# Kernel tuning notes

Hardware: AMD Instinct MI355X
Metric: run time of the kernel (lower is better)

## Reference

```python
import jax, jax.numpy as jnp
import numpy as np
import math

B, S, T = 32, 128, 64
FEAT = 16
H = 1024
V = 32000


def _gru_step(x, h, wih, whh, bih, bhh):
    # torch nn.GRU cell: gates ordered (r, z, n)
    gi = x @ wih.T + bih
    gh = h @ whh.T + bhh
    ir, iz, in_ = jnp.split(gi, 3, axis=-1)
    hr, hz, hn = jnp.split(gh, 3, axis=-1)
    r = jax.nn.sigmoid(ir + hr)
    z = jax.nn.sigmoid(iz + hz)
    n = jnp.tanh(in_ + r * hn)
    return (1.0 - z) * n + z * h


def _forward(features, target_tokens, temp_W, temp_b, hum_W, hum_b, cloud_W, cloud_b,
             time_W, time_b, other_W, other_b, fi_W, fi_b,
             enc_wih, enc_whh, enc_bih, enc_bhh, emb, attn_W, attn_b,
             dec_wih, dec_whh, dec_bih, dec_bhh, out_W, out_b):
    b = features.shape[0]
    # per-feature projections (dropout = identity in eval mode)
    temp = features[:, :, 0:1] @ temp_W.T + temp_b
    hum = features[:, :, 1:2] @ hum_W.T + hum_b
    cloud = features[:, :, 2:3] @ cloud_W.T + cloud_b
    time = features[:, :, -5:-3] @ time_W.T + time_b
    other_in = jnp.concatenate([features[:, :, 3:-5], features[:, :, -3:]], axis=2)
    other = other_in @ other_W.T + other_b
    concat = jnp.concatenate([temp, hum, cloud, time, other], axis=2)  # [B,S,2H]
    proj = jnp.tanh(concat @ fi_W.T + fi_b)  # [B,S,H]

    # encoder GRU over time
    def enc_step(h, x):
        h2 = _gru_step(x, h, enc_wih, enc_whh, enc_bih, enc_bhh)
        return h2, h2
    h0 = jnp.zeros((b, H), proj.dtype)
    h_last, enc_outs = jax.lax.scan(enc_step, h0, proj.transpose(1, 0, 2))
    enc_out = enc_outs.transpose(1, 0, 2)  # [B,S,H]

    # attention keys computed once (loop-invariant in the original)
    keys = enc_out @ attn_W.T + attn_b  # [B,S,H]
    scale = 1.0 / math.sqrt(H)

    # decoder: teacher_forcing_ratio = 1.0 -> input at step t is target_tokens[:, t-1]
    def dec_step(h, tok):
        e = emb[tok]  # [B,H]
        scores = jnp.einsum('bh,bsh->bs', h, keys) * scale
        w = jax.nn.softmax(scores, axis=-1)
        ctx = jnp.einsum('bs,bsh->bh', w, enc_out)
        x = jnp.concatenate([e, ctx], axis=-1)  # [B,2H]
        h2 = _gru_step(x, h, dec_wih, dec_whh, dec_bih, dec_bhh)
        pred = jnp.concatenate([h2, ctx], axis=-1) @ out_W.T + out_b  # [B,V]
        return h2, pred

    _, preds = jax.lax.scan(dec_step, h_last, target_tokens[:, :-1].T)  # [T-1,B,V]
    outputs = jnp.zeros((b, target_tokens.shape[1], V), preds.dtype)
    outputs = outputs.at[:, 0, target_tokens[0, 0]].set(1.0)
    outputs = outputs.at[:, 1:, :].set(preds.transpose(1, 0, 2))
    return outputs


def setup_inputs() -> dict:
    key = jax.random.key(0)
    ks = jax.random.split(key, 32)
    nrm = lambda k, sh: jax.random.normal(k, sh, jnp.float32) * 0.05
    Hq = H // 4
    d = {}
    d['features'] = jax.random.normal(ks[0], (B, S, FEAT), jnp.float32)
    d['target_tokens'] = jax.random.randint(ks[1], (B, T), 0, V, dtype=jnp.int32)
    d['temp_W'] = nrm(ks[2], (Hq, 1)); d['temp_b'] = nrm(ks[3], (Hq,))
    d['hum_W'] = nrm(ks[4], (Hq, 1)); d['hum_b'] = nrm(ks[5], (Hq,))
    d['cloud_W'] = nrm(ks[6], (Hq, 1)); d['cloud_b'] = nrm(ks[7], (Hq,))
    d['time_W'] = nrm(ks[8], (Hq, 2)); d['time_b'] = nrm(ks[9], (Hq,))
    d['other_W'] = nrm(ks[10], (H, FEAT - 5)); d['other_b'] = nrm(ks[11], (H,))
    d['fi_W'] = nrm(ks[12], (H, 2 * H)); d['fi_b'] = nrm(ks[13], (H,))
    d['enc_wih'] = nrm(ks[14], (3 * H, H)); d['enc_whh'] = nrm(ks[15], (3 * H, H))
    d['enc_bih'] = nrm(ks[16], (3 * H,)); d['enc_bhh'] = nrm(ks[17], (3 * H,))
    d['emb'] = nrm(ks[18], (V, H))
    d['attn_W'] = nrm(ks[19], (H, H)); d['attn_b'] = nrm(ks[20], (H,))
    d['dec_wih'] = nrm(ks[21], (3 * H, 2 * H)); d['dec_whh'] = nrm(ks[22], (3 * H, H))
    d['dec_bih'] = nrm(ks[23], (3 * H,)); d['dec_bhh'] = nrm(ks[24], (3 * H,))
    d['out_W'] = nrm(ks[25], (V, 2 * H)); d['out_b'] = nrm(ks[26], (V,))
    return d


def reference(features, target_tokens, temp_W, temp_b, hum_W, hum_b, cloud_W, cloud_b,
              time_W, time_b, other_W, other_b, fi_W, fi_b,
              enc_wih, enc_whh, enc_bih, enc_bhh, emb, attn_W, attn_b,
              dec_wih, dec_whh, dec_bih, dec_bhh, out_W, out_b):
    return _forward(features, target_tokens, temp_W, temp_b, hum_W, hum_b, cloud_W, cloud_b,
                    time_W, time_b, other_W, other_b, fi_W, fi_b,
                    enc_wih, enc_whh, enc_bih, enc_bhh, emb, attn_W, attn_b,
                    dec_wih, dec_whh, dec_bih, dec_bhh, out_W, out_b)
```

## Files before the change

### kernel.cpp

```cpp
#include <hip/hip_runtime.h>

typedef float f32x4 __attribute__((ext_vector_type(4)));
typedef __bf16 bf16x8 __attribute__((ext_vector_type(8)));

#define DI static __device__ __forceinline__

DI unsigned short f2bf(float f) {
  unsigned u = __float_as_uint(f);
  u = (u + 0x7fffu + ((u >> 16) & 1u)) >> 16;
  return (unsigned short)u;
}
DI unsigned pk2(float lo, float hi) {
  return (unsigned)f2bf(lo) | ((unsigned)f2bf(hi) << 16);
}
DI float bflo(unsigned u) { return __uint_as_float(u << 16); }
DI float bfhi(unsigned u) { return __uint_as_float(u & 0xffff0000u); }
DI float sigm(float x) { return 1.0f / (1.0f + expf(-x)); }

DI void gl_lds16(const unsigned short* g, unsigned short* l) {
  __builtin_amdgcn_global_load_lds(
      (const __attribute__((address_space(1))) unsigned int*)g,
      (__attribute__((address_space(3))) unsigned int*)l, 16, 0, 0);
}

DI void st32_sc1(unsigned* p, unsigned v) {
  __hip_atomic_store(p, v, __ATOMIC_RELAXED, __HIP_MEMORY_SCOPE_AGENT);
}
DI void st64_sc1(unsigned long long* p, unsigned long long v) {
  __hip_atomic_store(p, v, __ATOMIC_RELAXED, __HIP_MEMORY_SCOPE_AGENT);
}
DI int ldw(const int* p) {
  return __hip_atomic_load(p, __ATOMIC_RELAXED, __HIP_MEMORY_SCOPE_AGENT);
}
DI void stw(int* p, int v) {
  __hip_atomic_store(p, v, __ATOMIC_RELAXED, __HIP_MEMORY_SCOPE_AGENT);
}

DI void burn(int n) {
  float x = (float)(int)threadIdx.x;
#pragma unroll 1
  for (int i = 0; i < n; ++i) x = __builtin_fmaf(x, 1.0000001f, 1e-9f);
  asm volatile("" :: "v"(x));
}

DI void waitrel(const int* relbase, int repl, int target) {
  const int* w = relbase + repl * 32;
  for (;;) {
    int v = 0;
    if ((threadIdx.x & 63) == 0) v = ldw(w);
    v = __shfl(v, 0);
    if (v >= target) break;
    burn(60);
  }
  asm volatile("" ::: "memory");
}
DI void strel(int* relbase, int v) {
  int l = threadIdx.x & 63;
  if (l < 8) stw(relbase + l * 32, v);
}

__global__ void k_fold(const float* __restrict__ tW, const float* __restrict__ tb,
                       const float* __restrict__ hW, const float* __restrict__ hb,
                       const float* __restrict__ cW, const float* __restrict__ cb,
                       const float* __restrict__ tiW, const float* __restrict__ tib,
                       const float* __restrict__ oW, const float* __restrict__ ob,
                       const float* __restrict__ fiW, const float* __restrict__ fib,
                       float* __restrict__ M, float* __restrict__ b0v)
{
  int g = blockIdx.x * 256 + threadIdx.x;
  if (g >= 1024 * 17) return;
  int h = g / 17, f = g - h * 17;
  const float* fw = fiW + (size_t)h * 2048;
  float s = 0.f;
  if (f == 16) {
    for (int k = 0; k < 256; ++k) s += fw[k] * tb[k];
    for (int k = 0; k < 256; ++k) s += fw[256 + k] * hb[k];
    for (int k = 0; k < 256; ++k) s += fw[512 + k] * cb[k];
    for (int k = 0; k < 256; ++k) s += fw[768 + k] * tib[k];
    for (int r = 0; r < 1024; ++r) s += fw[1024 + r] * ob[r];
    b0v[h] = s + fib[h];
  } else if (f == 0) {
    for (int k = 0; k < 256; ++k) s += fw[k] * tW[k];
    M[h * 16 + 0] = s;
  } else if (f == 1) {
    for (int k = 0; k < 256; ++k) s += fw[256 + k] * hW[k];
    M[h * 16 + 1] = s;
  } else if (f == 2) {
    for (int k = 0; k < 256; ++k) s += fw[512 + k] * cW[k];
    M[h * 16 + 2] = s;
  } else if (f == 11) {
    for (int k = 0; k < 256; ++k) s += fw[768 + k] * tiW[2 * k];
    M[h * 16 + 11] = s;
  } else if (f == 12) {
    for (int k = 0; k < 256; ++k) s += fw[768 + k] * tiW[2 * k + 1];
    M[h * 16 + 12] = s;
  } else {
    int col = (f <= 10) ? (f - 3) : (f - 5);
    for (int r = 0; r < 1024; ++r) s += fw[1024 + r] * oW[r * 11 + col];
    M[h * 16 + f] = s;
  }
}

__global__ __launch_bounds__(256)
void k_proj(const float* __restrict__ feat, const float* __restrict__ M,
            const float* __restrict__ b0v, unsigned short* __restrict__ proj)
{
  __shared__ float ft[16];
  int bs = blockIdx.x;
  int h = blockIdx.y * 256 + threadIdx.x;
  if (threadIdx.x < 16) ft[threadIdx.x] = feat[bs * 16 + threadIdx.x];
  __syncthreads();
  float sum = b0v[h];
  const float* mr = M + h * 16;
#pragma unroll
  for (int f = 0; f < 16; ++f) sum += mr[f] * ft[f];
  proj[(size_t)bs * 1024 + h] = f2bf(tanhf(sum));
}

__global__ void k_conv(const float* __restrict__ s, unsigned short* __restrict__ d, int n8)
{
  for (long i = (long)blockIdx.x * 256 + threadIdx.x; i < n8; i += (long)gridDim.x * 256) {
    const float* p = s + i * 8;
    f32x4 a = *(const f32x4*)p, b = *(const f32x4*)(p + 4);
    uint4 o;
    o.x = pk2(a[0], a[1]); o.y = pk2(a[2], a[3]);
    o.z = pk2(b[0], b[1]); o.w = pk2(b[2], b[3]);
    *(uint4*)(d + i * 8) = o;
  }
}

__global__ void k_conv_str(const float* __restrict__ s, unsigned short* __restrict__ d, int coff)
{
  int r = blockIdx.x;
  int c = threadIdx.x * 4;
  f32x4 a = *(const f32x4*)(s + (size_t)r * 2048 + coff + c);
  uint2 o; o.x = pk2(a[0], a[1]); o.y = pk2(a[2], a[3]);
  *(uint2*)(d + (size_t)r * 1024 + c) = o;
}

__global__ void k_gather_e(const int* __restrict__ toks, const float* __restrict__ emb,
                           unsigned short* __restrict__ e_bf)
{
  int row = blockIdx.x;
  int t = row >> 5, b = row & 31;
  unsigned short* dst = e_bf + (size_t)row * 1024 + threadIdx.x * 4;
  if (t < 63) {
    int tok = toks[b * 64 + t];
    f32x4 a = *(const f32x4*)(emb + (size_t)tok * 1024 + threadIdx.x * 4);
    uint2 o; o.x = pk2(a[0], a[1]); o.y = pk2(a[2], a[3]);
    *(uint2*)dst = o;
  } else {
    uint2 o; o.x = 0u; o.y = 0u;
    *(uint2*)dst = o;
  }
}

__global__ void k_onehot(const int* __restrict__ toks, float* __restrict__ out)
{
  int i = blockIdx.x * 256 + threadIdx.x;
  if (i >= 32 * 32000) return;
  int b = i / 32000, v = i - b * 32000;
  out[(size_t)b * 64 * 32000 + v] = (v == toks[0]) ? 1.0f : 0.0f;
}

template<int MODE>
__global__ __launch_bounds__(256)
void gemm_bf(const unsigned short* __restrict__ A, const unsigned short* __restrict__ B,
             const float* __restrict__ bias, float* __restrict__ Cf,
             unsigned short* __restrict__ Cb,
             int tiles_m, int K, int lda, int ldb, int ldc, int coloff)
{
  __shared__ unsigned short As[4096];
  __shared__ unsigned short Bs[4096];
  const int nblk = gridDim.x;
  const int cpx = nblk >> 3;
  const int bid = blockIdx.x;
  const int id = (bid & 7) * cpx + (bid >> 3);
  const int tm = id % tiles_m, tn = id / tiles_m;
  const int tid = threadIdx.x;
  const int lane = tid & 63, wave = tid >> 6;
  const int wm = (wave & 1) << 6, wn = (wave >> 1) << 6;
  const int r0 = tid >> 2, kc0 = (tid & 3) << 3;
  const unsigned short* ga0 = A + (size_t)(tm * 128 + r0) * lda + kc0;
  const unsigned short* ga1 = A + (size_t)(tm * 128 + 64 + r0) * lda + kc0;
  const unsigned short* gb0 = B + (size_t)(tn * 128 + r0) * ldb + kc0;
  const unsigned short* gb1 = B + (size_t)(tn * 128 + 64 + r0) * ldb + kc0;
  const int lr = lane & 15, lkb = (lane >> 4) << 3;

  f32x4 acc[4][4];
#pragma unroll
  for (int m = 0; m < 4; ++m)
#pragma unroll
    for (int n = 0; n < 4; ++n) { acc[m][n][0]=0.f; acc[m][n][1]=0.f; acc[m][n][2]=0.f; acc[m][n][3]=0.f; }

  for (int kt = 0; kt < K; kt += 32) {
    __syncthreads();
    gl_lds16(ga0 + kt, &As[tid * 8]);
    gl_lds16(ga1 + kt, &As[(tid + 256) * 8]);
    gl_lds16(gb0 + kt, &Bs[tid * 8]);
    gl_lds16(gb1 + kt, &Bs[(tid + 256) * 8]);
    __syncthreads();
    bf16x8 af[4], bfv[4];
#pragma unroll
    for (int m = 0; m < 4; ++m) af[m] = *(const bf16x8*)&As[(wm + m * 16 + lr) * 32 + lkb];
#pragma unroll
    for (int n = 0; n < 4; ++n) bfv[n] = *(const bf16x8*)&Bs[(wn + n * 16 + lr) * 32 + lkb];
#pragma unroll
    for (int m = 0; m < 4; ++m)
#pragma unroll
      for (int n = 0; n < 4; ++n)
        acc[m][n] = __builtin_amdgcn_mfma_f32_16x16x32_bf16(af[m], bfv[n], acc[m][n], 0, 0, 0);
  }

#pragma unroll
  for (int m = 0; m < 4; ++m) {
    int rb = tm * 128 + wm + m * 16 + ((lane >> 4) << 2);
#pragma unroll
    for (int n = 0; n < 4; ++n) {
      int c = tn * 128 + wn + n * 16 + lr;
      float bb = bias[c];
#pragma unroll
      for (int i = 0; i < 4; ++i) {
        float v = acc[m][n][i] + bb;
        int r = rb + i;
        if (MODE == 0) {
          Cf[(size_t)r * ldc + c] = v;
        } else if (MODE == 1) {
          Cb[(size_t)r * ldc + c] = f2bf(v);
        } else if (MODE == 3) {
          Cb[(size_t)c * 4096 + r] = f2bf(v);
        } else {
          if (r < 2016) {
            int t = r >> 5, b2 = r & 31;
            Cf[((size_t)b2 * 64 + t + 1) * 32000 + coloff + c] = v;
          }
        }
      }
    }
  }
}

__global__ __launch_bounds__(256, 1)
void k_enc_scan(const float* __restrict__ gi_all, const float* __restrict__ whh,
                const float* __restrict__ bhh, float* __restrict__ hfp,
                unsigned short* __restrict__ enc_bf,
                int* __restrict__ arrE, int* __restrict__ relE)
{
  const int tid = threadIdx.x;
  const int blk = blockIdx.x;
  if (blk == 64) {
    if (tid < 64) {
      for (int g = 1; g <= 127; ++g) {
        for (;;) {
          int v = ldw(&arrE[tid << 3]);
          if (__all(v >= g)) break;
          burn(60);
        }
        asm volatile("" ::: "memory");
        strel(relE, g);
      }
    }
    return;
  }

  __shared__ unsigned short W[48 * 1024];
  __shared__ float Cred[4 * 2 * 3 * 64 * 4];
  const int lane = tid & 63, wave = tid >> 6;
  const int j0 = blk * 16;
  const int repl = blk & 7;

  for (int i = tid; i < 48 * 128; i += 256) {
    int r = i >> 7, c = i & 127;
    int gr = ((r >> 4) << 10) + j0 + (r & 15);
    const float* src = whh + ((size_t)gr << 10) + (c << 3);
    f32x4 a = *(const f32x4*)src, b = *(const f32x4*)(src + 4);
    uint4 o;
    o.x = pk2(a[0], a[1]); o.y = pk2(a[2], a[3]);
    o.z = pk2(b[0], b[1]); o.w = pk2(b[2], b[3]);
    *(uint4*)&W[(r << 10) + ((c ^ (r & 7)) << 3)] = o;
  }
  __syncthreads();

  int cb[2], cj[2], clb[2], creg[2], cm[2];
  float bh0[2], bh1[2], bh2[2];
  float hp[2] = {0.f, 0.f};
#pragma unroll
  for (int cc = 0; cc < 2; ++cc) {
    int cell = tid + (cc << 8);
    cb[cc] = cell >> 4; cj[cc] = cell & 15;
    clb[cc] = ((cb[cc] & 15) >> 2) * 16;
    creg[cc] = cb[cc] & 3; cm[cc] = cb[cc] >> 4;
    bh0[cc] = bhh[j0 + cj[cc]];
    bh1[cc] = bhh[1024 + j0 + cj[cc]];
    bh2[cc] = bhh[2048 + j0 + cj[cc]];
  }

#pragma unroll 1
  for (int s = 0; s < 128; ++s) {
    float gp[2][3];
#pragma unroll
    for (int cc = 0; cc < 2; ++cc) {
      const float* gi = gi_all + ((size_t)cb[cc] * 128 + s) * 3072 + j0 + cj[cc];
      gp[cc][0] = gi[0]; gp[cc][1] = gi[1024]; gp[cc][2] = gi[2048];
    }

    f32x4 acc[2][3];
#pragma unroll
    for (int m = 0; m < 2; ++m)
#pragma unroll
      for (int n = 0; n < 3; ++n) { acc[m][n][0]=0.f; acc[m][n][1]=0.f; acc[m][n][2]=0.f; acc[m][n][3]=0.f; }

    if (s > 0) {
      waitrel(relE, repl, s);
      const unsigned short* hr = enc_bf + (size_t)(s - 1) * 1024;
      const int k0 = wave << 8;
      bf16x8 af[2][8];
#pragma unroll
      for (int kk = 0; kk < 8; ++kk) {
        int k = k0 + kk * 32 + ((lane >> 4) << 3);
        af[0][kk] = *(const bf16x8*)(hr + (size_t)(lane & 15) * 131072 + k);
        af[1][kk] = *(const bf16x8*)(hr + (size_t)(16 + (lane & 15)) * 131072 + k);
      }
#pragma unroll
      for (int kk = 0; kk < 8; ++kk) {
        int c = ((k0 + kk * 32) >> 3) + (lane >> 4);
#pragma unroll
        for (int n = 0; n < 3; ++n) {
          int wr = n * 16 + (lane & 15);
          bf16x8 bfr = *(const bf16x8*)&W[(wr << 10) + ((c ^ (wr & 7)) << 3)];
          acc[0][n] = __builtin_amdgcn_mfma_f32_16x16x32_bf16(af[0][kk], bfr, acc[0][n], 0, 0, 0);
          acc[1][n] = __builtin_amdgcn_mfma_f32_16x16x32_bf16(af[1][kk], bfr, acc[1][n], 0, 0, 0);
        }
      }
    }
#pragma unroll
    for (int m = 0; m < 2; ++m)
#pragma unroll
      for (int n = 0; n < 3; ++n)
        *(f32x4*)&Cred[((((wave * 2 + m) * 3 + n) * 64) + lane) << 2] = acc[m][n];
    __syncthreads();

    float h2v[2];
#pragma unroll
    for (int cc = 0; cc < 2; ++cc) {
      int lj = clb[cc] + cj[cc], reg = creg[cc], m = cm[cc];
      float Cr = 0.f, Cz = 0.f, Cn = 0.f;
#pragma unroll
      for (int w = 0; w < 4; ++w) {
        Cr += Cred[((((w * 2 + m) * 3 + 0) * 64 + lj) << 2) + reg];
        Cz += Cred[((((w * 2 + m) * 3 + 1) * 64 + lj) << 2) + reg];
        Cn += Cred[((((w * 2 + m) * 3 + 2) * 64 + lj) << 2) + reg];
      }
      float r = sigm(gp[cc][0] + Cr + bh0[cc]);
      float z = sigm(gp[cc][1] + Cz + bh1[cc]);
      float n = tanhf(gp[cc][2] + r * (Cn + bh2[cc]));
      float h2 = (1.f - z) * n + z * hp[cc];
      h2v[cc] = h2; hp[cc] = h2;
    }
    if (s == 127) {
      hfp[cb[0] * 1024 + j0 + cj[0]] = h2v[0];
      hfp[cb[1] * 1024 + j0 + cj[1]] = h2v[1];
    }
#pragma unroll
    for (int cc = 0; cc < 2; ++cc) {
      unsigned short sv = f2bf(h2v[cc]);
      unsigned p = (unsigned)sv | (((unsigned)__shfl_xor((int)(unsigned)sv, 1)) << 16);
      unsigned q = (unsigned)__shfl_xor((int)p, 2);
      if ((tid & 3) == 0) {
        unsigned long long dv = (unsigned long long)p | ((unsigned long long)q << 32);
        st64_sc1((unsigned long long*)&enc_bf[((size_t)cb[cc] * 128 + s) * 1024 + j0 + cj[cc]], dv);
      }
    }
    __syncthreads();
    if (tid == 0) stw(&arrE[blk << 3], s + 1);
  }
}

__global__ __launch_bounds__(256, 1)
void k_dec_scan(const float* __restrict__ gi_e, const float* __restrict__ whh,
                const float* __restrict__ bhh,
                const unsigned short* __restrict__ keys,
                const unsigned short* __restrict__ enc_bf,
                unsigned short* __restrict__ hcat, const float* __restrict__ hfp0,
                const unsigned short* __restrict__ xeT, float* __restrict__ w_all,
                int* __restrict__ arrW, int* __restrict__ arrH,
                int* __restrict__ relD)
{
  static __shared__ __attribute__((aligned(16))) char smem[135168];
  const int tid = threadIdx.x;
  const int blk = blockIdx.x;
  const int repl = blk & 7;

  if (blk == 192) {
    if (tid < 64) {
      for (int t = 0; t < 63; ++t) {
        for (;;) {
          int v = ldw(&arrW[tid << 3]);
          if (__all(v >= t + 1)) break;
          burn(60);
        }
        asm volatile("" ::: "memory");
        strel(relD, 2 * t + 1);
        for (;;) {
          int v0 = ldw(&arrH[(tid * 2) << 4]);
          int v1 = ldw(&arrH[(tid * 2 + 1) << 4]);
          if (__all(v0 >= t + 1 && v1 >= t + 1)) break;
          burn(60);
        }
        asm volatile("" ::: "memory");
        strel(relD, 2 * t + 2);
      }
    }
    return;
  }

  if (blk < 64) {
    unsigned short* Ks = (unsigned short*)smem;
    unsigned short* hsh = (unsigned short*)(smem + 131072);
    float* parr = (float*)(smem + 133120);
    const int b = blk >> 1, half = blk & 1;
    const int lane = tid & 63, wave = tid >> 6;

    for (int i = tid; i < 64 * 128; i += 256) {
      int s = i >> 7, c = i & 127;
      uint4 kv = *(const uint4*)(keys + ((size_t)(b * 128 + half * 64 + s) << 10) + (c << 3));
      *(uint4*)&Ks[(s << 10) + ((c ^ (s & 7)) << 3)] = kv;
    }
    __syncthreads();

#pragma unroll 1
    for (int t = 0; t < 63; ++t) {
      if (t) waitrel(relD, repl, 2 * t);
      const unsigned short* hsrc = (t == 0)
          ? (enc_bf + (size_t)b * 131072 + (size_t)127 * 1024)
          : (hcat + ((size_t)(t - 1) * 32 + b) * 2048);
      *(uint2*)&hsh[tid * 4] = *(const uint2*)(hsrc + tid * 4);
      __syncthreads();
      float a0 = 0.f, a1 = 0.f;
#pragma unroll 8
      for (int i = 0; i < 32; i += 2) {
        int c0 = wave * 32 + i, c1 = c0 + 1;
        uint4 kv0 = *(const uint4*)&Ks[(lane << 10) + ((c0 ^ (lane & 7)) << 3)];
        uint4 kv1 = *(const uint4*)&Ks[(lane << 10) + ((c1 ^ (lane & 7)) << 3)];
        uint4 hv0 = *(const uint4*)&hsh[c0 << 3];
        uint4 hv1 = *(const uint4*)&hsh[c1 << 3];
        a0 += bflo(kv0.x) * bflo(hv0.x) + bfhi(kv0.x) * bfhi(hv0.x)
            + bflo(kv0.y) * bflo(hv0.y) + bfhi(kv0.y) * bfhi(hv0.y)
            + bflo(kv0.z) * bflo(hv0.z) + bfhi(kv0.z) * bfhi(hv0.z)
            + bflo(kv0.w) * bflo(hv0.w) + bfhi(kv0.w) * bfhi(hv0.w);
        a1 += bflo(kv1.x) * bflo(hv1.x) + bfhi(kv1.x) * bfhi(hv1.x)
            + bflo(kv1.y) * bflo(hv1.y) + bfhi(kv1.y) * bfhi(hv1.y)
            + bflo(kv1.z) * bflo(hv1.z) + bfhi(kv1.z) * bfhi(hv1.z)
            + bflo(kv1.w) * bflo(hv1.w) + bfhi(kv1.w) * bfhi(hv1.w);
      }
      parr[wave * 64 + lane] = a0 + a1;
      __syncthreads();
      if (tid < 64) {
        float sc = (parr[tid] + parr[64 + tid] + parr[128 + tid] + parr[192 + tid]) * 0.03125f;
        float e = expf(sc);
        float eo = __shfl_xor(e, 1);
        if ((tid & 1) == 0) {
          unsigned long long dv = (unsigned long long)__float_as_uint(e)
                                | ((unsigned long long)__float_as_uint(eo) << 32);
          st64_sc1((unsigned long long*)(w_all + ((size_t)t * 32 + b) * 128 + half * 64 + tid), dv);
        }
      }
      __syncthreads();
      if (tid == 0) stw(&arrW[blk << 3], t + 1);
    }
    return;
  }

  unsigned short* Wh = (unsigned short*)smem;
  float* Cred = (float*)(smem + 65536);
  const int lane = tid & 63, wave = tid >> 6;
  const int gblk = blk - 64;
  const int j0 = gblk * 8;

  for (int i = tid; i < 32 * 128; i += 256) {
    int r = i >> 7, c = i & 127;
    int off = (r << 10) + ((c ^ (r & 7)) << 3);
    uint4 oh;
    oh.x = oh.y = oh.z = oh.w = 0u;
    if (r < 24) {
      int gr = ((r >> 3) << 10) + j0 + (r & 7);
      const float* sh = whh + ((size_t)gr << 10) + (c << 3);
      f32x4 a = *(const f32x4*)sh, b = *(const f32x4*)(sh + 4);
      oh.x = pk2(a[0], a[1]); oh.y = pk2(a[2], a[3]);
      oh.z = pk2(b[0], b[1]); oh.w = pk2(b[2], b[3]);
    }
    *(uint4*)&Wh[off] = oh;
  }
  __syncthreads();

  const int gb = tid >> 3, gj = tid & 7;
  const int glb = ((gb & 15) >> 2) * 16;
  const int greg = gb & 3, gm = gb >> 4;
  const float bh0 = bhh[j0 + gj];
  const float bh1 = bhh[1024 + j0 + gj];
  const float bh2 = bhh[2048 + j0 + gj];
  float hpv = hfp0[gb * 1024 + j0 + gj];

  uint4 x0v[16], x1v[16], x2v[16];
  {
    const unsigned short* x0 = xeT + ((size_t)(j0 + gj) << 12) + gb * 128;
    const unsigned short* x1 = xeT + ((size_t)(1024 + j0 + gj) << 12) + gb * 128;
    const unsigned short* x2 = xeT + ((size_t)(2048 + j0 + gj) << 12) + gb * 128;
#pragma unroll
    for (int i = 0; i < 16; ++i) {
      x0v[i] = *(const uint4*)(x0 + i * 8);
      x1v[i] = *(const uint4*)(x1 + i * 8);
      x2v[i] = *(const uint4*)(x2 + i * 8);
    }
  }

#pragma unroll 1
  for (int t = 0; t < 63; ++t) {
    const float* gie = gi_e + ((size_t)t * 32 + gb) * 3072 + j0 + gj;
    float g0 = gie[0], g1 = gie[1024], g2 = gie[2048];

    if (t) waitrel(relD, repl, 2 * t);
    const unsigned short* abase;
    size_t astr;
    if (t == 0) { abase = enc_bf + (size_t)127 * 1024; astr = 131072; }
    else { abase = hcat + (size_t)(t - 1) * 32 * 2048; astr = 2048; }
    const int k0 = wave << 8;
    f32x4 acc[2][2];
#pragma unroll
    for (int m = 0; m < 2; ++m)
#pragma unroll
      for (int n = 0; n < 2; ++n) { acc[m][n][0]=0.f; acc[m][n][1]=0.f; acc[m][n][2]=0.f; acc[m][n][3]=0.f; }
    {
      bf16x8 af[2][8];
#pragma unroll
      for (int kk = 0; kk < 8; ++kk) {
        int k = k0 + kk * 32 + ((lane >> 4) << 3);
        af[0][kk] = *(const bf16x8*)(abase + (size_t)(lane & 15) * astr + k);
        af[1][kk] = *(const bf16x8*)(abase + (size_t)(16 + (lane & 15)) * astr + k);
      }
#pragma unroll
      for (int kk = 0; kk < 8; ++kk) {
        int c = ((k0 + kk * 32) >> 3) + (lane >> 4);
#pragma unroll
        for (int n = 0; n < 2; ++n) {
          int wr = n * 16 + (lane & 15);
          bf16x8 bfr = *(const bf16x8*)&Wh[(wr << 10) + ((c ^ (wr & 7)) << 3)];
          acc[0][n] = __builtin_amdgcn_mfma_f32_16x16x32_bf16(af[0][kk], bfr, acc[0][n], 0, 0, 0);
          acc[1][n] = __builtin_amdgcn_mfma_f32_16x16x32_bf16(af[1][kk], bfr, acc[1][n], 0, 0, 0);
        }
      }
    }
#pragma unroll
    for (int m = 0; m < 2; ++m)
#pragma unroll
      for (int n = 0; n < 2; ++n)
        *(f32x4*)&Cred[((((wave * 2 + m) * 2 + n) * 64) + lane) << 2] = acc[m][n];
    __syncthreads();

    waitrel(relD, repl, 2 * t + 1);
    const float* wrow = w_all + ((size_t)t * 32 + gb) * 128;
    float se = 0.f, cx0 = 0.f, cx1 = 0.f, cx2 = 0.f;
#pragma unroll
    for (int i = 0; i < 16; ++i) {
      f32x4 wa = *(const f32x4*)(wrow + i * 8);
      f32x4 wb2 = *(const f32x4*)(wrow + i * 8 + 4);
      se += (wa[0] + wa[1]) + (wa[2] + wa[3]) + (wb2[0] + wb2[1]) + (wb2[2] + wb2[3]);
      uint4 a0 = x0v[i], a1 = x1v[i], a2 = x2v[i];
      cx0 += wa[0]*bflo(a0.x) + wa[1]*bfhi(a0.x) + wa[2]*bflo(a0.y) + wa[3]*bfhi(a0.y)
           + wb2[0]*bflo(a0.z) + wb2[1]*bfhi(a0.z) + wb2[2]*bflo(a0.w) + wb2[3]*bfhi(a0.w);
      cx1 += wa[0]*bflo(a1.x) + wa[1]*bfhi(a1.x) + wa[2]*bflo(a1.y) + wa[3]*bfhi(a1.y)
           + wb2[0]*bflo(a1.z) + wb2[1]*bfhi(a1.z) + wb2[2]*bflo(a1.w) + wb2[3]*bfhi(a1.w);
      cx2 += wa[0]*bflo(a2.x) + wa[1]*bfhi(a2.x) + wa[2]*bflo(a2.y) + wa[3]*bfhi(a2.y)
           + wb2[0]*bflo(a2.z) + wb2[1]*bfhi(a2.z) + wb2[2]*bflo(a2.w) + wb2[3]*bfhi(a2.w);
    }
    float inv = 1.f / se;
    cx0 *= inv; cx1 *= inv; cx2 *= inv;

    {
      float Chr = 0.f, Chz = 0.f, Chn = 0.f;
#pragma unroll
      for (int w = 0; w < 4; ++w) {
        Chr += Cred[((((w * 2 + gm) * 2 + 0) * 64 + glb + gj) << 2) + greg];
        Chz += Cred[((((w * 2 + gm) * 2 + 0) * 64 + glb + gj + 8) << 2) + greg];
        Chn += Cred[((((w * 2 + gm) * 2 + 1) * 64 + glb + gj) << 2) + greg];
      }
      float r = sigm(g0 + cx0 + Chr + bh0);
      float z = sigm(g1 + cx1 + Chz + bh1);
      float n2 = tanhf(g2 + cx2 + r * (Chn + bh2));
      float h2 = (1.f - z) * n2 + z * hpv;
      hpv = h2;
      unsigned short sv = f2bf(h2);
      unsigned p = (unsigned)sv | (((unsigned)__shfl_xor((int)(unsigned)sv, 1)) << 16);
      unsigned q = (unsigned)__shfl_xor((int)p, 2);
      if ((tid & 3) == 0) {
        unsigned long long dv = (unsigned long long)p | ((unsigned long long)q << 32);
        st64_sc1((unsigned long long*)&hcat[((size_t)t * 32 + gb) * 2048 + j0 + gj], dv);
      }
    }
    __syncthreads();
    if (tid == 0) stw(&arrH[gblk << 4], t + 1);
  }
}

__global__ __launch_bounds__(256)
void k_ctx(const float* __restrict__ w_all, const unsigned short* __restrict__ enc_bf,
           unsigned short* __restrict__ hcat)
{
  __shared__ float wsh[8][128];
  __shared__ float inv[8];
  const int b = blockIdx.x, tg = blockIdx.y;
  const int t0 = tg * 8;
  const int nt = (t0 + 8 <= 63) ? 8 : (63 - t0);
  const int tid = threadIdx.x;
  for (int idx = tid; idx < 8 * 128; idx += 256) {
    int tt = idx >> 7, s = idx & 127;
    wsh[tt][s] = (tt < nt) ? w_all[((size_t)(t0 + tt) * 32 + b) * 128 + s] : 0.f;
  }
  __syncthreads();
  if (tid < 8) {
    float s = 0.f;
    for (int i = 0; i < 128; ++i) s += wsh[tid][i];
    inv[tid] = (tid < nt) ? 1.f / s : 0.f;
  }
  __syncthreads();
  const int j0 = tid * 4;
  f32x4 cacc[8];
#pragma unroll
  for (int tt = 0; tt < 8; ++tt) { cacc[tt][0]=0.f; cacc[tt][1]=0.f; cacc[tt][2]=0.f; cacc[tt][3]=0.f; }
  const unsigned short* eb = enc_bf + ((size_t)b << 17) + j0;
  for (int s = 0; s < 128; ++s) {
    uint2 ev = *(const uint2*)(eb + ((size_t)s << 10));
    float v0 = bflo(ev.x), v1 = bfhi(ev.x), v2 = bflo(ev.y), v3 = bfhi(ev.y);
#pragma unroll
    for (int tt = 0; tt < 8; ++tt) {
      float w = wsh[tt][s];
      cacc[tt][0] += w * v0; cacc[tt][1] += w * v1;
      cacc[tt][2] += w * v2; cacc[tt][3] += w * v3;
    }
  }
#pragma unroll
  for (int tt = 0; tt < 8; ++tt) {
    if (tt < nt) {
      float iv = inv[tt];
      uint2 co;
      co.x = pk2(cacc[tt][0] * iv, cacc[tt][1] * iv);
      co.y = pk2(cacc[tt][2] * iv, cacc[tt][3] * iv);
      *(uint2*)(hcat + ((size_t)(t0 + tt) * 32 + b) * 2048 + 1024 + j0) = co;
    }
  }
}

extern "C" void kernel_launch(void* const* d_in, const int* in_sizes, int n_in,
                              void* d_out, int out_size, void* d_ws, size_t ws_size,
                              hipStream_t stream)
{
  const float* features = (const float*)d_in[0];
  const int*   toks     = (const int*)d_in[1];
  const float* temp_W = (const float*)d_in[2];  const float* temp_b = (const float*)d_in[3];
  const float* hum_W  = (const float*)d_in[4];  const float* hum_b  = (const float*)d_in[5];
  const float* cloud_W= (const float*)d_in[6];  const float* cloud_b= (const float*)d_in[7];
  const float* time_W = (const float*)d_in[8];  const float* time_b = (const float*)d_in[9];
  const float* other_W= (const float*)d_in[10]; const float* other_b= (const float*)d_in[11];
  const float* fi_W   = (const float*)d_in[12]; const float* fi_b   = (const float*)d_in[13];
  const float* enc_wih= (const float*)d_in[14]; const float* enc_whh= (const float*)d_in[15];
  const float* enc_bih= (const float*)d_in[16]; const float* enc_bhh= (const float*)d_in[17];
  const float* emb    = (const float*)d_in[18];
  const float* attn_W = (const float*)d_in[19]; const float* attn_b = (const float*)d_in[20];
  const float* dec_wih= (const float*)d_in[21]; const float* dec_whh= (const float*)d_in[22];
  const float* dec_bih= (const float*)d_in[23]; const float* dec_bhh= (const float*)d_in[24];
  const float* out_W  = (const float*)d_in[25]; const float* out_b  = (const float*)d_in[26];
  float* out = (float*)d_out;
  char* ws = (char*)d_ws;

  int*            arrE    = (int*)(ws + 0);
  int*            arrH    = (int*)(ws + 4096);
  int*            arrW    = (int*)(ws + 12288);
  int*            relE    = (int*)(ws + 14336);
  int*            relD    = (int*)(ws + 15360);
  float*          zbias   = (float*)(ws + 16384);
  float*          Mf      = (float*)(ws + 32768);
  float*          b0v     = (float*)(ws + 98304);
  float*          hfp     = (float*)(ws + 102400);
  unsigned short* hcat    = (unsigned short*)(ws + 233472);
  unsigned short* keys_bf = (unsigned short*)(ws + 8622080);
  unsigned short* enc_bf  = (unsigned short*)(ws + 17010688);
  float*          w_all   = (float*)(ws + 25399296);
  float*          gi_e    = (float*)(ws + 26447872);
  unsigned short* xeT     = (unsigned short*)(ws + 51613696);
  float*          gi_all  = (float*)(ws + 76779520);
  unsigned short* proj_bf = (unsigned short*)(ws + 127111168);
  unsigned short* e_bf    = (unsigned short*)(ws + 135499776);
  unsigned short* wihE_bf = (unsigned short*)(ws + 139694080);
  unsigned short* attnW_bf= (unsigned short*)(ws + 145985536);
  unsigned short* wihD_bf = (unsigned short*)(ws + 148082688);
  unsigned short* wihDc_bf= (unsigned short*)(ws + 154374144);
  unsigned short* outW_bf = (unsigned short*)(ws + 26447872);

  hipMemsetAsync(ws, 0, 32768, stream);
  hipMemsetAsync(ws + 233472 + (size_t)2016 * 2048 * 2, 0, 32 * 2048 * 2, stream);

  k_conv<<<1536, 256, 0, stream>>>(enc_wih, wihE_bf, 393216);
  k_conv<<<512, 256, 0, stream>>>(attn_W, attnW_bf, 131072);
  k_conv_str<<<3072, 256, 0, stream>>>(dec_wih, wihD_bf, 0);
  k_conv_str<<<3072, 256, 0, stream>>>(dec_wih, wihDc_bf, 1024);

  k_fold<<<68, 256, 0, stream>>>(temp_W, temp_b, hum_W, hum_b, cloud_W, cloud_b,
                                 time_W, time_b, other_W, other_b, fi_W, fi_b, Mf, b0v);
  k_proj<<<dim3(4096, 4), 256, 0, stream>>>(features, Mf, b0v, proj_bf);

  gemm_bf<0><<<768, 256, 0, stream>>>(proj_bf, wihE_bf, enc_bih, gi_all, nullptr,
                                      32, 1024, 1024, 1024, 3072, 0);
  k_enc_scan<<<65, 256, 0, stream>>>(gi_all, enc_whh, enc_bhh, hfp, enc_bf, arrE, relE);

  gemm_bf<1><<<256, 256, 0, stream>>>(enc_bf, attnW_bf, attn_b, nullptr, keys_bf,
                                      32, 1024, 1024, 1024, 1024, 0);
  k_gather_e<<<2048, 256, 0, stream>>>(toks, emb, e_bf);
  gemm_bf<0><<<384, 256, 0, stream>>>(e_bf, wihD_bf, dec_bih, gi_e, nullptr,
                                      16, 1024, 1024, 1024, 3072, 0);
  gemm_bf<3><<<768, 256, 0, stream>>>(enc_bf, wihDc_bf, zbias, nullptr, xeT,
                                      32, 1024, 1024, 1024, 0, 0);
  k_dec_scan<<<193, 256, 0, stream>>>(gi_e, dec_whh, dec_bhh, keys_bf, enc_bf,
                                      hcat, hfp, xeT, w_all, arrW, arrH, relD);
  k_ctx<<<dim3(32, 8), 256, 0, stream>>>(w_all, enc_bf, hcat);

  k_conv<<<2048, 256, 0, stream>>>(out_W, outW_bf, 4096000);
  gemm_bf<2><<<2000, 256, 0, stream>>>(hcat, outW_bf, out_b, out, nullptr,
                                       16, 2048, 2048, 2048, 0, 0);
  k_conv<<<2048, 256, 0, stream>>>(out_W + (size_t)16000 * 2048, outW_bf, 4096000);
  gemm_bf<2><<<2000, 256, 0, stream>>>(hcat, outW_bf, out_b + 16000, out, nullptr,
                                       16, 2048, 2048, 2048, 0, 16000);
  k_onehot<<<4000, 256, 0, stream>>>(toks, out);
}
```

Baseline: 2.617 ms.

## Replace coordinator-block barriers with atomic-counter last-arriver release in scans

The dedicated coordinator block in the encoder and decoder scan kernels is removed. Each block now atomically increments a per-step counter, and the last block to arrive publishes the release flag to the eight replicas. The decoder's single interleaved release word is split into two separate flags, one for attention weights and one for the hidden state. The spin-wait is simplified so every thread polls directly, with a shorter multi-chain burn loop. This is meant to cut one polling hop of latency per step and free a workgroup, at the cost of atomic contention on the counters. It also drops one __syncthreads after the shared h load, which could introduce a race.

After: 2.752 ms. 1.05x slower.

```diff
diff --git a/kernel.cpp b/kernel.cpp
--- a/kernel.cpp
+++ b/kernel.cpp
@@ -23,9 +23,6 @@
       (__attribute__((address_space(3))) unsigned int*)l, 16, 0, 0);
 }
 
-DI void st32_sc1(unsigned* p, unsigned v) {
-  __hip_atomic_store(p, v, __ATOMIC_RELAXED, __HIP_MEMORY_SCOPE_AGENT);
-}
 DI void st64_sc1(unsigned long long* p, unsigned long long v) {
   __hip_atomic_store(p, v, __ATOMIC_RELAXED, __HIP_MEMORY_SCOPE_AGENT);
 }
@@ -36,27 +33,31 @@
   __hip_atomic_store(p, v, __ATOMIC_RELAXED, __HIP_MEMORY_SCOPE_AGENT);
 }
 
-DI void burn(int n) {
-  float x = (float)(int)threadIdx.x;
+DI void burn4(int n) {
+  float x0 = 1.f + (float)(int)threadIdx.x, x1 = 2.f, x2 = 3.f, x3 = 4.f;
 #pragma unroll 1
-  for (int i = 0; i < n; ++i) x = __builtin_fmaf(x, 1.0000001f, 1e-9f);
-  asm volatile("" :: "v"(x));
-}
-
-DI void waitrel(const int* relbase, int repl, int target) {
+  for (int i = 0; i < n; ++i) {
+    x0 = __builtin_fmaf(x0, 1.0000001f, 1e-9f);
+    x1 = __builtin_fmaf(x1, 1.0000001f, 2e-9f);
+    x2 = __builtin_fmaf(x2, 1.0000001f, 3e-9f);
+    x3 = __builtin_fmaf(x3, 1.0000001f, 4e-9f);
+  }
+  asm volatile("" :: "v"(x0), "v"(x1), "v"(x2), "v"(x3));
+}
+
+DI void waitrel2(const int* relbase, int repl, int target) {
   const int* w = relbase + repl * 32;
-  for (;;) {
-    int v = 0;
-    if ((threadIdx.x & 63) == 0) v = ldw(w);
-    v = __shfl(v, 0);
-    if (v >= target) break;
-    burn(60);
-  }
+  while (ldw(w) < target) burn4(40);
   asm volatile("" ::: "memory");
 }
-DI void strel(int* relbase, int v) {
-  int l = threadIdx.x & 63;
-  if (l < 8) stw(relbase + l * 32, v);
+DI void arrive_release(int* cnt, int nblk, int* relbase, int relval) {
+  if (threadIdx.x == 0) {
+    int old = __hip_atomic_fetch_add(cnt, 1, __ATOMIC_RELAXED, __HIP_MEMORY_SCOPE_AGENT);
+    if (old == nblk - 1) {
+#pragma unroll
+      for (int i = 0; i < 8; ++i) stw(relbase + i * 32, relval);
+    }
+  }
 }
 
 __global__ void k_fold(const float* __restrict__ tW, const float* __restrict__ tb,
@@ -244,24 +245,10 @@
 void k_enc_scan(const float* __restrict__ gi_all, const float* __restrict__ whh,
                 const float* __restrict__ bhh, float* __restrict__ hfp,
                 unsigned short* __restrict__ enc_bf,
-                int* __restrict__ arrE, int* __restrict__ relE)
+                int* __restrict__ cntE, int* __restrict__ relE)
 {
   const int tid = threadIdx.x;
   const int blk = blockIdx.x;
-  if (blk == 64) {
-    if (tid < 64) {
-      for (int g = 1; g <= 127; ++g) {
-        for (;;) {
-          int v = ldw(&arrE[tid << 3]);
-          if (__all(v >= g)) break;
-          burn(60);
-        }
-        asm volatile("" ::: "memory");
-        strel(relE, g);
-      }
-    }
-    return;
-  }
 
   __shared__ unsigned short W[48 * 1024];
   __shared__ float Cred[4 * 2 * 3 * 64 * 4];
@@ -311,7 +298,7 @@
       for (int n = 0; n < 3; ++n) { acc[m][n][0]=0.f; acc[m][n][1]=0.f; acc[m][n][2]=0.f; acc[m][n][3]=0.f; }
 
     if (s > 0) {
-      waitrel(relE, repl, s);
+      waitrel2(relE, repl, s);
       const unsigned short* hr = enc_bf + (size_t)(s - 1) * 1024;
       const int k0 = wave << 8;
       bf16x8 af[2][8];
@@ -372,7 +359,7 @@
       }
     }
     __syncthreads();
-    if (tid == 0) stw(&arrE[blk << 3], s + 1);
+    arrive_release(&cntE[s << 4], 64, relE, s + 1);
   }
 }
 
@@ -383,36 +370,13 @@
                 const unsigned short* __restrict__ enc_bf,
                 unsigned short* __restrict__ hcat, const float* __restrict__ hfp0,
                 const unsigned short* __restrict__ xeT, float* __restrict__ w_all,
-                int* __restrict__ arrW, int* __restrict__ arrH,
-                int* __restrict__ relD)
+                int* __restrict__ cntW, int* __restrict__ cntH,
+                int* __restrict__ relDe, int* __restrict__ relDh)
 {
   static __shared__ __attribute__((aligned(16))) char smem[135168];
   const int tid = threadIdx.x;
   const int blk = blockIdx.x;
   const int repl = blk & 7;
-
-  if (blk == 192) {
-    if (tid < 64) {
-      for (int t = 0; t < 63; ++t) {
-        for (;;) {
-          int v = ldw(&arrW[tid << 3]);
-          if (__all(v >= t + 1)) break;
-          burn(60);
-        }
-        asm volatile("" ::: "memory");
-        strel(relD, 2 * t + 1);
-        for (;;) {
-          int v0 = ldw(&arrH[(tid * 2) << 4]);
-          int v1 = ldw(&arrH[(tid * 2 + 1) << 4]);
-          if (__all(v0 >= t + 1 && v1 >= t + 1)) break;
-          burn(60);
-        }
-        asm volatile("" ::: "memory");
-        strel(relD, 2 * t + 2);
-      }
-    }
-    return;
-  }
 
   if (blk < 64) {
     unsigned short* Ks = (unsigned short*)smem;
@@ -430,12 +394,11 @@
 
 #pragma unroll 1
     for (int t = 0; t < 63; ++t) {
-      if (t) waitrel(relD, repl, 2 * t);
+      if (t) waitrel2(relDh, repl, t);
       const unsigned short* hsrc = (t == 0)
           ? (enc_bf + (size_t)b * 131072 + (size_t)127 * 1024)
           : (hcat + ((size_t)(t - 1) * 32 + b) * 2048);
       *(uint2*)&hsh[tid * 4] = *(const uint2*)(hsrc + tid * 4);
-      __syncthreads();
       float a0 = 0.f, a1 = 0.f;
 #pragma unroll 8
       for (int i = 0; i < 32; i += 2) {
@@ -466,7 +429,7 @@
         }
       }
       __syncthreads();
-      if (tid == 0) stw(&arrW[blk << 3], t + 1);
+      arrive_release(&cntW[t << 4], 64, relDe, t + 1);
     }
     return;
   }
@@ -519,7 +482,7 @@
     const float* gie = gi_e + ((size_t)t * 32 + gb) * 3072 + j0 + gj;
     float g0 = gie[0], g1 = gie[1024], g2 = gie[2048];
 
-    if (t) waitrel(relD, repl, 2 * t);
+    if (t) waitrel2(relDh, repl, t);
     const unsigned short* abase;
     size_t astr;
     if (t == 0) { abase = enc_bf + (size_t)127 * 1024; astr = 131072; }
@@ -557,7 +520,7 @@
         *(f32x4*)&Cred[((((wave * 2 + m) * 2 + n) * 64) + lane) << 2] = acc[m][n];
     __syncthreads();
 
-    waitrel(relD, repl, 2 * t + 1);
+    waitrel2(relDe, repl, t + 1);
     const float* wrow = w_all + ((size_t)t * 32 + gb) * 128;
     float se = 0.f, cx0 = 0.f, cx1 = 0.f, cx2 = 0.f;
 #pragma unroll
@@ -598,7 +561,7 @@
       }
     }
     __syncthreads();
-    if (tid == 0) stw(&arrH[gblk << 4], t + 1);
+    arrive_release(&cntH[t << 4], 128, relDh, t + 1);
   }
 }
 
@@ -672,12 +635,13 @@
   float* out = (float*)d_out;
   char* ws = (char*)d_ws;
 
-  int*            arrE    = (int*)(ws + 0);
-  int*            arrH    = (int*)(ws + 4096);
-  int*            arrW    = (int*)(ws + 12288);
-  int*            relE    = (int*)(ws + 14336);
-  int*            relD    = (int*)(ws + 15360);
-  float*          zbias   = (float*)(ws + 16384);
+  int*            cntE    = (int*)(ws + 0);
+  int*            cntW    = (int*)(ws + 8192);
+  int*            cntH    = (int*)(ws + 12288);
+  int*            relE    = (int*)(ws + 16384);
+  int*            relDe   = (int*)(ws + 17408);
+  int*            relDh   = (int*)(ws + 18432);
+  float*          zbias   = (float*)(ws + 20480);
   float*          Mf      = (float*)(ws + 32768);
   float*          b0v     = (float*)(ws + 98304);
   float*          hfp     = (float*)(ws + 102400);
@@ -710,7 +674,7 @@
 
   gemm_bf<0><<<768, 256, 0, stream>>>(proj_bf, wihE_bf, enc_bih, gi_all, nullptr,
                                       32, 1024, 1024, 1024, 3072, 0);
-  k_enc_scan<<<65, 256, 0, stream>>>(gi_all, enc_whh, enc_bhh, hfp, enc_bf, arrE, relE);
+  k_enc_scan<<<64, 256, 0, stream>>>(gi_all, enc_whh, enc_bhh, hfp, enc_bf, cntE, relE);
 
   gemm_bf<1><<<256, 256, 0, stream>>>(enc_bf, attnW_bf, attn_b, nullptr, keys_bf,
                                       32, 1024, 1024, 1024, 1024, 0);
@@ -719,8 +683,8 @@
                                       16, 1024, 1024, 1024, 3072, 0);
   gemm_bf<3><<<768, 256, 0, stream>>>(enc_bf, wihDc_bf, zbias, nullptr, xeT,
                                       32, 1024, 1024, 1024, 0, 0);
-  k_dec_scan<<<193, 256, 0, stream>>>(gi_e, dec_whh, dec_bhh, keys_bf, enc_bf,
-                                      hcat, hfp, xeT, w_all, arrW, arrH, relD);
+  k_dec_scan<<<192, 256, 0, stream>>>(gi_e, dec_whh, dec_bhh, keys_bf, enc_bf,
+                                      hcat, hfp, xeT, w_all, cntW, cntH, relDe, relDh);
   k_ctx<<<dim3(32, 8), 256, 0, stream>>>(w_all, enc_bf, hcat);
 
   k_conv<<<2048, 256, 0, stream>>>(out_W, outW_bf, 4096000);
```
